# Kernel optimization log

Measured on AMD Instinct MI355X. Metric: run time of the kernel, lower is better.

Reference implementation:

```python
import jax, jax.numpy as jnp
import numpy as np

B, S, D, H, O = 128, 512, 128, 1024, 64
IN = 2 * D + 1  # input_size*2 + 1


def _xavier(key, shape):
    fan_out, fan_in = shape
    std = np.sqrt(2.0 / (fan_in + fan_out)).astype(np.float32)
    return jax.random.normal(key, shape, jnp.float32) * std


def setup_inputs() -> dict:
    key = jax.random.key(0)
    ks = jax.random.split(key, 6)
    x = jax.random.normal(ks[0], (B, S, D), jnp.float32)
    mask = jax.random.uniform(ks[1], (B, S, D), jnp.float32)
    ti = jax.random.uniform(ks[2], (B, S, 1), jnp.float32)
    W_ih = _xavier(ks[3], (4 * H, IN))   # LSTMCell weight_ih
    W_hh = _xavier(ks[4], (4 * H, H))    # LSTMCell weight_hh
    b_ih = jnp.zeros((4 * H,), jnp.float32)
    b_hh = jnp.zeros((4 * H,), jnp.float32)
    W_fc = _xavier(ks[5], (O, H))
    b_fc = jnp.zeros((O,), jnp.float32)
    return {"x": x, "mask": mask, "ti": ti, "W_ih": W_ih, "W_hh": W_hh,
            "b_ih": b_ih, "b_hh": b_hh, "W_fc": W_fc, "b_fc": b_fc}


def reference(x, mask, ti, W_ih, W_hh, b_ih, b_hh, W_fc, b_fc):
    b, s, _ = x.shape
    h = W_hh.shape[1]
    xt = jnp.concatenate([x, mask, ti], axis=-1)          # [B,S,IN]
    # Precompute input contribution to gates for all timesteps (one big GEMM)
    xg = jnp.einsum('bsi,gi->sbg', xt, W_ih) + b_ih + b_hh  # [S,B,4H]

    def step(carry, xg_t):
        h_t, c_t = carry
        g = xg_t + h_t @ W_hh.T                             # [B,4H]
        i, f, gg, o = jnp.split(g, 4, axis=-1)              # torch gate order i,f,g,o
        i = jax.nn.sigmoid(i)
        f = jax.nn.sigmoid(f)
        gg = jnp.tanh(gg)
        o = jax.nn.sigmoid(o)
        c_new = f * c_t + i * gg
        h_new = o * jnp.tanh(c_new)
        return (h_new, c_new), None

    h0 = jnp.zeros((b, h), x.dtype)
    c0 = jnp.zeros((b, h), x.dtype)
    (h_last, _), _ = jax.lax.scan(step, (h0, c0), xg)
    return h_last @ W_fc.T + b_fc                           # [B,O]
```

## Files before the change

### kernel.cpp

```cpp
#include <hip/hip_runtime.h>
#include <hip/hip_bf16.h>

typedef __bf16 bf16x8 __attribute__((ext_vector_type(8)));
typedef float f32x4 __attribute__((ext_vector_type(4)));
typedef unsigned int u32x4 __attribute__((ext_vector_type(4)));

#define BB   128
#define SS   512
#define DD   128
#define HH   1024
#define OO   64
#define IIN  257

#define NGROUP 8
#define GBLK   64
#define MG     16
#define KK_H   32
#define KK_X   9

#define XTP_TP    (KK_X*512)
#define HBUF_SLAB (KK_H*512)
#define WIH_BLK   (4*KK_X*512)

#define WS_HBUF  8192
#define WS_HLAST 532480
#define WS_XTP   1056768
#define WS_WIHP  38805504

__device__ __forceinline__ u32x4 ldg_dev16(const void* p) {
  u32x4 r;
  asm volatile("global_load_dwordx4 %0, %1, off sc1" : "=v"(r) : "v"(p));
  return r;
}
__device__ __forceinline__ void stg_dev4(void* p, unsigned int v) {
  asm volatile("global_store_dword %0, %1, off sc1" :: "v"(p), "v"(v));
}
__device__ __forceinline__ bf16x8 asbf(u32x4 v) {
  union { u32x4 u; bf16x8 h; } c; c.u = v; return c.h;
}

#define CLAIMW4(CNTSTR, A, O)                                        \
  asm volatile("s_waitcnt vmcnt(" CNTSTR ")"                         \
    : "+v"((A)[(O)]), "+v"((A)[(O)+1]), "+v"((A)[(O)+2]), "+v"((A)[(O)+3]))

__global__ void prepack_kernel(const float* __restrict__ x, const float* __restrict__ mask,
                               const float* __restrict__ ti, __bf16* __restrict__ xtp) {
  int idx = blockIdx.x * 256 + threadIdx.x;
  int j = idx & 7, l = (idx >> 3) & 63;
  int rest = idx >> 9;
  int kk = rest % 9;
  int rest2 = rest / 9;
  int p = rest2 & 7;
  int t = rest2 >> 3;
  int b = p * MG + (l & 15);
  int k = kk * 32 + ((l >> 4) << 3) + j;
  float v;
  if (k < 128)       v = x[(b * SS + t) * DD + k];
  else if (k < 256)  v = mask[(b * SS + t) * DD + (k - 128)];
  else if (k == 256) v = ti[b * SS + t];
  else               v = 0.f;
  xtp[idx] = (__bf16)v;
}

__global__ void wih_prepack(const float* __restrict__ W_ih, __bf16* __restrict__ wihp) {
  int idx = blockIdx.x * 256 + threadIdx.x;
  int j = idx & 7, l = (idx >> 3) & 63;
  int rest = idx >> 9;
  int kk = rest % 9;
  int rest2 = rest / 9;
  int nt = rest2 & 3, q = rest2 >> 2;
  int col = nt * HH + q * 16 + (l & 15);
  int k = kk * 32 + ((l >> 4) << 3) + j;
  wihp[idx] = (k < IIN) ? (__bf16)W_ih[col * IIN + k] : (__bf16)0.f;
}

__device__ __forceinline__ float sigmoid_f(float v) { return 1.f / (1.f + __expf(-v)); }
__device__ __forceinline__ float tanh_f(float v)    { return 1.f - 2.f / (__expf(2.f * v) + 1.f); }

__launch_bounds__(256, 2)
__global__ void lstm_scan(const float* __restrict__ W_hh,
                          const float* __restrict__ b_ih, const float* __restrict__ b_hh,
                          const __bf16* __restrict__ xtp, const __bf16* __restrict__ wihp,
                          __bf16* __restrict__ hbuf,
                          float* __restrict__ hlast, unsigned int* __restrict__ flags) {
  __shared__ float red_lds[8192];

  const int tid = threadIdx.x;
  const int bid = blockIdx.x;
  const int p = bid >> 6;
  const int q = bid & 63;
  const int j0 = q * 16;

  const int w = tid >> 6, l = tid & 63;
  const int n16 = l & 15, qh = l >> 4;
  unsigned int* gflags = flags + p * 256;

  bf16x8 breg[4][8];
  #pragma unroll
  for (int ntI = 0; ntI < 4; ++ntI) {
    const float* wrow = W_hh + (size_t)(ntI * HH + j0 + n16) * HH;
    #pragma unroll
    for (int i = 0; i < 8; ++i) {
      const float* src = wrow + (w * 8 + i) * 32 + qh * 8;
      bf16x8 bv;
      #pragma unroll
      for (int jj = 0; jj < 8; ++jj) bv[jj] = (__bf16)src[jj];
      breg[ntI][i] = bv;
    }
  }

  const int grow = qh * 4 + w;
  float bias_r[4];
  #pragma unroll
  for (int g = 0; g < 4; ++g)
    bias_r[g] = b_ih[g * HH + j0 + n16] + b_hh[g * HH + j0 + n16];
  float creg = 0.f;

  const int xs = (w == 0) ? 0 : (2 * w + 1);
  const int xe = xs + ((w == 0) ? 3 : 2);

  for (int t = 0; t < SS; ++t) {
    const int rb = t & 1, wb = rb ^ 1;
    f32x4 acc[4];
    #pragma unroll
    for (int ntI = 0; ntI < 4; ++ntI) acc[ntI] = (f32x4){0.f, 0.f, 0.f, 0.f};

    for (int kk = xs; kk < xe; ++kk) {
      const __bf16* xb = xtp + ((size_t)(t * 8 + p) * KK_X + kk) * 512 + l * 8;
      bf16x8 a = *(const bf16x8*)xb;
      #pragma unroll
      for (int ntI = 0; ntI < 4; ++ntI) {
        bf16x8 b = *(const bf16x8*)(wihp + ((size_t)(q * 4 + ntI) * KK_X + kk) * 512 + l * 8);
        acc[ntI] = __builtin_amdgcn_mfma_f32_16x16x32_bf16(a, b, acc[ntI], 0, 0, 0);
      }
    }

    if (t > 0) {
      if (tid < 64) {
        const unsigned int tgt = (unsigned int)t;
        for (;;) {
          u32x4 f4;
          asm volatile("global_load_dwordx4 %0, %1, off sc1\n\t"
                       "s_waitcnt vmcnt(0)"
                       : "=v"(f4) : "v"(gflags + tid * 4));
          if (!__ballot(f4[0] < tgt || f4[1] < tgt || f4[2] < tgt || f4[3] < tgt)) break;
          __builtin_amdgcn_s_sleep(1);
        }
      }
      __syncthreads();
    }

    {
      const __bf16* hbL = hbuf + (p * 2 + rb) * HBUF_SLAB + (w * 8) * 512 + l * 8;
      u32x4 A[8];
      #pragma unroll
      for (int i = 0; i < 8; ++i) A[i] = ldg_dev16(hbL + i * 512);

      CLAIMW4("4", A, 0);
      #pragma unroll
      for (int i = 0; i < 4; ++i)
        #pragma unroll
        for (int ntI = 0; ntI < 4; ++ntI)
          acc[ntI] = __builtin_amdgcn_mfma_f32_16x16x32_bf16(asbf(A[i]), breg[ntI][i], acc[ntI], 0, 0, 0);
      CLAIMW4("0", A, 4);
      #pragma unroll
      for (int i = 4; i < 8; ++i)
        #pragma unroll
        for (int ntI = 0; ntI < 4; ++ntI)
          acc[ntI] = __builtin_amdgcn_mfma_f32_16x16x32_bf16(asbf(A[i]), breg[ntI][i], acc[ntI], 0, 0, 0);
    }

    #pragma unroll
    for (int g = 0; g < 4; ++g)
      #pragma unroll
      for (int r = 0; r < 4; ++r)
        red_lds[(((w * 4 + g) * 4 + r) * 4 + qh) * 32 + n16 * 2 + (qh & 1)] = acc[g][r];
    __syncthreads();

    {
      __bf16* hw = hbuf + (p * 2 + wb) * HBUF_SLAB;
      float gv[4];
      #pragma unroll
      for (int g = 0; g < 4; ++g) {
        float own = (w == 0) ? acc[g][0] : (w == 1) ? acc[g][1]
                  : (w == 2) ? acc[g][2] : acc[g][3];
        float s = own + bias_r[g];
        #pragma unroll
        for (int wo = 0; wo < 4; ++wo)
          if (wo != w)
            s += red_lds[(((wo * 4 + g) * 4 + w) * 4 + qh) * 32 + n16 * 2 + (qh & 1)];
        gv[g] = s;
      }
      float i_ = sigmoid_f(gv[0]);
      float f_ = sigmoid_f(gv[1]);
      float g_ = tanh_f(gv[2]);
      float o_ = sigmoid_f(gv[3]);
      float c  = f_ * creg + i_ * g_;
      creg = c;
      float h  = o_ * tanh_f(c);

      union { __bf16 b; unsigned short u; } cv; cv.b = (__bf16)h;
      unsigned int hu = (unsigned int)cv.u;
      unsigned int partner = __shfl_xor(hu, 1);
      if ((n16 & 1) == 0) {
        unsigned int dw = hu | (partner << 16);
        int k = j0 + n16;
        int kk = k >> 5, q2 = (k >> 3) & 3, jj = k & 7;
        stg_dev4(hw + kk * 512 + (q2 * 16 + grow) * 8 + jj, dw);
      }
      if (t == SS - 1) hlast[(p * MG + grow) * HH + j0 + n16] = h;
    }

    asm volatile("s_waitcnt vmcnt(0)" ::: "memory");
    if (t < SS - 1 && l == 0) {
      stg_dev4(gflags + q * 4 + w, (unsigned int)(t + 1));
    }
  }
}

__global__ void fc_kernel(const float* __restrict__ hlast, const float* __restrict__ W_fc,
                          const float* __restrict__ b_fc, float* __restrict__ out) {
  int b = blockIdx.x;
  int t = threadIdx.x;
  int o = t >> 2, part = t & 3;
  const float* hr = hlast + b * HH;
  const float* wr = W_fc + o * HH;
  float s = 0.f;
  #pragma unroll 4
  for (int k0 = part * 4; k0 < HH; k0 += 16) {
    float4 hv = *(const float4*)(hr + k0);
    float4 wv = *(const float4*)(wr + k0);
    s += hv.x * wv.x + hv.y * wv.y + hv.z * wv.z + hv.w * wv.w;
  }
  s += __shfl_xor(s, 1);
  s += __shfl_xor(s, 2);
  if (part == 0) out[b * OO + o] = s + b_fc[o];
}

extern "C" void kernel_launch(void* const* d_in, const int* in_sizes, int n_in,
                              void* d_out, int out_size, void* d_ws, size_t ws_size,
                              hipStream_t stream) {
  const float* x    = (const float*)d_in[0];
  const float* mask = (const float*)d_in[1];
  const float* ti   = (const float*)d_in[2];
  const float* W_ih = (const float*)d_in[3];
  const float* W_hh = (const float*)d_in[4];
  const float* b_ih = (const float*)d_in[5];
  const float* b_hh = (const float*)d_in[6];
  const float* W_fc = (const float*)d_in[7];
  const float* b_fc = (const float*)d_in[8];
  float* out = (float*)d_out;

  char* ws = (char*)d_ws;
  unsigned int* flags = (unsigned int*)ws;
  __bf16* hbuf  = (__bf16*)(ws + WS_HBUF);
  float*  hlast = (float*)(ws + WS_HLAST);
  __bf16* xtp   = (__bf16*)(ws + WS_XTP);
  __bf16* wihp  = (__bf16*)(ws + WS_WIHP);

  hipMemsetAsync(ws, 0, WS_HLAST, stream);

  prepack_kernel<<<(SS * NGROUP * XTP_TP) / 256, 256, 0, stream>>>(x, mask, ti, xtp);
  wih_prepack<<<(GBLK * WIH_BLK) / 256, 256, 0, stream>>>(W_ih, wihp);
  lstm_scan<<<NGROUP * GBLK, 256, 0, stream>>>(W_hh, b_ih, b_hh, xtp, wihp, hbuf, hlast, flags);
  fc_kernel<<<BB, 256, 0, stream>>>(hlast, W_fc, b_fc, out);
}
```

Measured before the change: 2.173 ms.

## Halve scan workgroups by giving each block 32 hidden units with one flag

Each persistent scan block now owns 32 hidden columns, so every wave carries 8 gate tiles of W_hh in registers instead of 4. Launch bounds drop to one block per CU and the LDS reduction buffer doubles. Per-wave completion flags become a single per-block flag written after a block barrier, and the poll reads one dword per lane without sleeping. The aim is to cut the number of blocks that must synchronise each timestep and the flag-polling traffic, at the cost of more registers per block, longer per-step MFMA chains and an extra barrier.

```diff
diff --git a/kernel.cpp b/kernel.cpp
--- a/kernel.cpp
+++ b/kernel.cpp
@@ -13,14 +13,15 @@
 #define IIN  257
 
 #define NGROUP 8
-#define GBLK   64
+#define GBLK   32
 #define MG     16
+#define NTT    8
 #define KK_H   32
 #define KK_X   9
 
 #define XTP_TP    (KK_X*512)
 #define HBUF_SLAB (KK_H*512)
-#define WIH_BLK   (4*KK_X*512)
+#define WIH_BLK   (NTT*KK_X*512)
 
 #define WS_HBUF  8192
 #define WS_HLAST 532480
@@ -68,8 +69,8 @@
   int rest = idx >> 9;
   int kk = rest % 9;
   int rest2 = rest / 9;
-  int nt = rest2 & 3, q = rest2 >> 2;
-  int col = nt * HH + q * 16 + (l & 15);
+  int nt = rest2 & 7, q = rest2 >> 3;
+  int col = (nt >> 1) * HH + q * 32 + (nt & 1) * 16 + (l & 15);
   int k = kk * 32 + ((l >> 4) << 3) + j;
   wihp[idx] = (k < IIN) ? (__bf16)W_ih[col * IIN + k] : (__bf16)0.f;
 }
@@ -77,28 +78,28 @@
 __device__ __forceinline__ float sigmoid_f(float v) { return 1.f / (1.f + __expf(-v)); }
 __device__ __forceinline__ float tanh_f(float v)    { return 1.f - 2.f / (__expf(2.f * v) + 1.f); }
 
-__launch_bounds__(256, 2)
+__launch_bounds__(256, 1)
 __global__ void lstm_scan(const float* __restrict__ W_hh,
                           const float* __restrict__ b_ih, const float* __restrict__ b_hh,
                           const __bf16* __restrict__ xtp, const __bf16* __restrict__ wihp,
                           __bf16* __restrict__ hbuf,
                           float* __restrict__ hlast, unsigned int* __restrict__ flags) {
-  __shared__ float red_lds[8192];
+  __shared__ float red_lds[16384];
 
   const int tid = threadIdx.x;
   const int bid = blockIdx.x;
-  const int p = bid >> 6;
-  const int q = bid & 63;
-  const int j0 = q * 16;
+  const int p = bid >> 5;
+  const int q = bid & 31;
+  const int j0 = q * 32;
 
   const int w = tid >> 6, l = tid & 63;
   const int n16 = l & 15, qh = l >> 4;
-  unsigned int* gflags = flags + p * 256;
-
-  bf16x8 breg[4][8];
+  unsigned int* gflags = flags + p * 32;
+
+  bf16x8 breg[NTT][8];
   #pragma unroll
-  for (int ntI = 0; ntI < 4; ++ntI) {
-    const float* wrow = W_hh + (size_t)(ntI * HH + j0 + n16) * HH;
+  for (int ntI = 0; ntI < NTT; ++ntI) {
+    const float* wrow = W_hh + (size_t)((ntI >> 1) * HH + j0 + (ntI & 1) * 16 + n16) * HH;
     #pragma unroll
     for (int i = 0; i < 8; ++i) {
       const float* src = wrow + (w * 8 + i) * 32 + qh * 8;
@@ -110,27 +111,29 @@
   }
 
   const int grow = qh * 4 + w;
-  float bias_r[4];
+  float bias_r[4][2];
   #pragma unroll
   for (int g = 0; g < 4; ++g)
-    bias_r[g] = b_ih[g * HH + j0 + n16] + b_hh[g * HH + j0 + n16];
-  float creg = 0.f;
+    #pragma unroll
+    for (int s = 0; s < 2; ++s)
+      bias_r[g][s] = b_ih[g * HH + j0 + s * 16 + n16] + b_hh[g * HH + j0 + s * 16 + n16];
+  float creg[2] = {0.f, 0.f};
 
   const int xs = (w == 0) ? 0 : (2 * w + 1);
   const int xe = xs + ((w == 0) ? 3 : 2);
 
   for (int t = 0; t < SS; ++t) {
     const int rb = t & 1, wb = rb ^ 1;
-    f32x4 acc[4];
-    #pragma unroll
-    for (int ntI = 0; ntI < 4; ++ntI) acc[ntI] = (f32x4){0.f, 0.f, 0.f, 0.f};
+    f32x4 acc[NTT];
+    #pragma unroll
+    for (int ntI = 0; ntI < NTT; ++ntI) acc[ntI] = (f32x4){0.f, 0.f, 0.f, 0.f};
 
     for (int kk = xs; kk < xe; ++kk) {
       const __bf16* xb = xtp + ((size_t)(t * 8 + p) * KK_X + kk) * 512 + l * 8;
       bf16x8 a = *(const bf16x8*)xb;
       #pragma unroll
-      for (int ntI = 0; ntI < 4; ++ntI) {
-        bf16x8 b = *(const bf16x8*)(wihp + ((size_t)(q * 4 + ntI) * KK_X + kk) * 512 + l * 8);
+      for (int ntI = 0; ntI < NTT; ++ntI) {
+        bf16x8 b = *(const bf16x8*)(wihp + ((size_t)(q * NTT + ntI) * KK_X + kk) * 512 + l * 8);
         acc[ntI] = __builtin_amdgcn_mfma_f32_16x16x32_bf16(a, b, acc[ntI], 0, 0, 0);
       }
     }
@@ -139,12 +142,11 @@
       if (tid < 64) {
         const unsigned int tgt = (unsigned int)t;
         for (;;) {
-          u32x4 f4;
-          asm volatile("global_load_dwordx4 %0, %1, off sc1\n\t"
+          unsigned int fa;
+          asm volatile("global_load_dword %0, %1, off sc1\n\t"
                        "s_waitcnt vmcnt(0)"
-                       : "=v"(f4) : "v"(gflags + tid * 4));
-          if (!__ballot(f4[0] < tgt || f4[1] < tgt || f4[2] < tgt || f4[3] < tgt)) break;
-          __builtin_amdgcn_s_sleep(1);
+                       : "=v"(fa) : "v"(gflags + (tid & 31)));
+          if (!__ballot(fa < tgt)) break;
         }
       }
       __syncthreads();
@@ -160,60 +162,69 @@
       #pragma unroll
       for (int i = 0; i < 4; ++i)
         #pragma unroll
-        for (int ntI = 0; ntI < 4; ++ntI)
+        for (int ntI = 0; ntI < NTT; ++ntI)
           acc[ntI] = __builtin_amdgcn_mfma_f32_16x16x32_bf16(asbf(A[i]), breg[ntI][i], acc[ntI], 0, 0, 0);
       CLAIMW4("0", A, 4);
       #pragma unroll
       for (int i = 4; i < 8; ++i)
         #pragma unroll
-        for (int ntI = 0; ntI < 4; ++ntI)
+        for (int ntI = 0; ntI < NTT; ++ntI)
           acc[ntI] = __builtin_amdgcn_mfma_f32_16x16x32_bf16(asbf(A[i]), breg[ntI][i], acc[ntI], 0, 0, 0);
     }
 
     #pragma unroll
-    for (int g = 0; g < 4; ++g)
+    for (int ntI = 0; ntI < NTT; ++ntI)
       #pragma unroll
       for (int r = 0; r < 4; ++r)
-        red_lds[(((w * 4 + g) * 4 + r) * 4 + qh) * 32 + n16 * 2 + (qh & 1)] = acc[g][r];
+        red_lds[(((w * 8 + ntI) * 4 + r) * 4 + qh) * 32 + n16 * 2 + (qh & 1)] = acc[ntI][r];
     __syncthreads();
 
     {
       __bf16* hw = hbuf + (p * 2 + wb) * HBUF_SLAB;
-      float gv[4];
-      #pragma unroll
-      for (int g = 0; g < 4; ++g) {
-        float own = (w == 0) ? acc[g][0] : (w == 1) ? acc[g][1]
-                  : (w == 2) ? acc[g][2] : acc[g][3];
-        float s = own + bias_r[g];
+      float h2[2];
+      #pragma unroll
+      for (int s = 0; s < 2; ++s) {
+        float gv[4];
         #pragma unroll
-        for (int wo = 0; wo < 4; ++wo)
-          if (wo != w)
-            s += red_lds[(((wo * 4 + g) * 4 + w) * 4 + qh) * 32 + n16 * 2 + (qh & 1)];
-        gv[g] = s;
-      }
-      float i_ = sigmoid_f(gv[0]);
-      float f_ = sigmoid_f(gv[1]);
-      float g_ = tanh_f(gv[2]);
-      float o_ = sigmoid_f(gv[3]);
-      float c  = f_ * creg + i_ * g_;
-      creg = c;
-      float h  = o_ * tanh_f(c);
-
-      union { __bf16 b; unsigned short u; } cv; cv.b = (__bf16)h;
-      unsigned int hu = (unsigned int)cv.u;
-      unsigned int partner = __shfl_xor(hu, 1);
-      if ((n16 & 1) == 0) {
-        unsigned int dw = hu | (partner << 16);
-        int k = j0 + n16;
-        int kk = k >> 5, q2 = (k >> 3) & 3, jj = k & 7;
-        stg_dev4(hw + kk * 512 + (q2 * 16 + grow) * 8 + jj, dw);
-      }
-      if (t == SS - 1) hlast[(p * MG + grow) * HH + j0 + n16] = h;
+        for (int g = 0; g < 4; ++g) {
+          int nt = g * 2 + s;
+          float own = (w == 0) ? acc[nt][0] : (w == 1) ? acc[nt][1]
+                    : (w == 2) ? acc[nt][2] : acc[nt][3];
+          float sum = own + bias_r[g][s];
+          #pragma unroll
+          for (int wo = 0; wo < 4; ++wo)
+            if (wo != w)
+              sum += red_lds[(((wo * 8 + nt) * 4 + w) * 4 + qh) * 32 + n16 * 2 + (qh & 1)];
+          gv[g] = sum;
+        }
+        float i_ = sigmoid_f(gv[0]);
+        float f_ = sigmoid_f(gv[1]);
+        float g_ = tanh_f(gv[2]);
+        float o_ = sigmoid_f(gv[3]);
+        float c  = f_ * creg[s] + i_ * g_;
+        creg[s] = c;
+        h2[s] = o_ * tanh_f(c);
+      }
+      #pragma unroll
+      for (int s = 0; s < 2; ++s) {
+        union { __bf16 b; unsigned short u; } cv; cv.b = (__bf16)h2[s];
+        unsigned int hu = (unsigned int)cv.u;
+        unsigned int partner = __shfl_xor(hu, 1);
+        if ((n16 & 1) == 0) {
+          unsigned int dw = hu | (partner << 16);
+          int k = j0 + s * 16 + n16;
+          int kk = k >> 5, q2 = (k >> 3) & 3, jj = k & 7;
+          stg_dev4(hw + kk * 512 + (q2 * 16 + grow) * 8 + jj, dw);
+        }
+        if (t == SS - 1)
+          hlast[(p * MG + grow) * HH + j0 + s * 16 + n16] = h2[s];
+      }
     }
 
     asm volatile("s_waitcnt vmcnt(0)" ::: "memory");
-    if (t < SS - 1 && l == 0) {
-      stg_dev4(gflags + q * 4 + w, (unsigned int)(t + 1));
+    __syncthreads();
+    if (t < SS - 1 && tid == 0) {
+      stg_dev4(gflags + q, (unsigned int)(t + 1));
     }
   }
 }
```

Measured after the change: 3.698 ms. 1.7x slower.
